# Performance work log

Hardware: AMD Instinct MI355X
Metric: run time of the kernel (lower is better)

Reference implementation:

```python
import jax, jax.numpy as jnp
import numpy as np

C = 256
HEADS = 4
HIDDEN = 4 * C  # LeFF default hidden_dim = dim*4
EPS = 1e-5


def conv2d(x, w, pad):
    # x: [B,C,H,W], w: [O,I,kh,kw]
    return jax.lax.conv_general_dilated(
        x, w, window_strides=(1, 1), padding=[(pad, pad), (pad, pad)],
        dimension_numbers=('NCHW', 'OIHW', 'NCHW'))


def dwconv2d(x, w, pad):
    # depthwise: w: [C,1,kh,kw], groups = C
    return jax.lax.conv_general_dilated(
        x, w, window_strides=(1, 1), padding=[(pad, pad), (pad, pad)],
        dimension_numbers=('NCHW', 'OIHW', 'NCHW'),
        feature_group_count=x.shape[1])


def conv1x1(x, w):
    # w: [O, I]; pointwise conv as einsum
    return jnp.einsum('oi,bihw->bohw', w, x)


def layernorm(x, weight, bias):
    # WithBias LayerNorm over channel dim of NCHW (matches to_3d -> LN over c)
    mu = jnp.mean(x, axis=1, keepdims=True)
    var = jnp.mean((x - mu) ** 2, axis=1, keepdims=True)
    xn = (x - mu) / jnp.sqrt(var + EPS)
    return xn * weight[None, :, None, None] + bias[None, :, None, None]


def mhsa(q, k, v, heads):
    # q,k,v: [B,C,H,W] -> global attention over N = H*W tokens
    b, c, h, w = q.shape
    d = c // heads
    scale = d ** -0.5
    def split(t):
        return t.reshape(b, heads, d, h * w)  # [B,H,d,N]
    qh, kh, vh = split(q), split(k), split(v)
    attn = jnp.einsum('bhdn,bhdm->bhnm', qh, kh) * scale  # [B,H,N,N]
    attn = jax.nn.softmax(attn, axis=-1)
    out = jnp.einsum('bhnm,bhdm->bhdn', attn, vh)
    return out.reshape(b, c, h, w)


def self_attn(x, w_qkv, w_proj, heads):
    qkv = conv1x1(x, w_qkv)  # [B,3C,H,W]
    q, k, v = jnp.split(qkv, 3, axis=1)
    return conv1x1(mhsa(q, k, v, heads), w_proj)


def cross_attn(qf, kvf, w_q, w_k, w_v, w_proj, heads):
    q = conv1x1(qf, w_q)
    k = conv1x1(kvf, w_k)
    v = conv1x1(kvf, w_v)
    return conv1x1(mhsa(q, k, v, heads), w_proj)


def leff(x, w_in, w_dw, w_out):
    h = conv1x1(x, w_in)
    h = dwconv2d(h, w_dw, pad=1)
    h = jax.nn.gelu(h, approximate=False)  # torch nn.GELU() = exact erf
    return conv1x1(h, w_out)


def setup_inputs() -> dict:
    key = jax.random.key(0)
    ks = jax.random.split(key, 32)
    s = 0.02
    inp = {
        'aop_feat': jax.random.normal(ks[0], (8, C, 32, 32), jnp.float32),
        'dop_feat': jax.random.normal(ks[1], (8, C, 32, 32), jnp.float32),
        'w_qconv': jax.random.normal(ks[2], (C, C, 3, 3), jnp.float32) * s,
        'w_kvconv': jax.random.normal(ks[3], (C, C, 5, 5), jnp.float32) * s,
        'lnq1_w': jnp.ones((C,), jnp.float32), 'lnq1_b': jnp.zeros((C,), jnp.float32),
        'lnkv1_w': jnp.ones((C,), jnp.float32), 'lnkv1_b': jnp.zeros((C,), jnp.float32),
        'lnq2_w': jnp.ones((C,), jnp.float32), 'lnq2_b': jnp.zeros((C,), jnp.float32),
        'lnkv2_w': jnp.ones((C,), jnp.float32), 'lnkv2_b': jnp.zeros((C,), jnp.float32),
        'lnffn_w': jnp.ones((C,), jnp.float32), 'lnffn_b': jnp.zeros((C,), jnp.float32),
        'saq_qkv': jax.random.normal(ks[4], (3 * C, C), jnp.float32) * s,
        'saq_proj': jax.random.normal(ks[5], (C, C), jnp.float32) * s,
        'sakv_qkv': jax.random.normal(ks[6], (3 * C, C), jnp.float32) * s,
        'sakv_proj': jax.random.normal(ks[7], (C, C), jnp.float32) * s,
        'ca_q': jax.random.normal(ks[8], (C, C), jnp.float32) * s,
        'ca_k': jax.random.normal(ks[9], (C, C), jnp.float32) * s,
        'ca_v': jax.random.normal(ks[10], (C, C), jnp.float32) * s,
        'ca_proj': jax.random.normal(ks[11], (C, C), jnp.float32) * s,
        'leff_in': jax.random.normal(ks[12], (HIDDEN, C), jnp.float32) * s,
        'leff_dw': jax.random.normal(ks[13], (HIDDEN, 1, 3, 3), jnp.float32) * s,
        'leff_out': jax.random.normal(ks[14], (C, HIDDEN), jnp.float32) * s,
    }
    return inp


def reference(aop_feat, dop_feat, w_qconv, w_kvconv,
              lnq1_w, lnq1_b, lnkv1_w, lnkv1_b, lnq2_w, lnq2_b,
              lnkv2_w, lnkv2_b, lnffn_w, lnffn_b,
              saq_qkv, saq_proj, sakv_qkv, sakv_proj,
              ca_q, ca_k, ca_v, ca_proj,
              leff_in, leff_dw, leff_out):
    # q branch
    q_branch = conv2d(aop_feat, w_qconv, pad=1)
    q_branch = q_branch + self_attn(layernorm(q_branch, lnq1_w, lnq1_b), saq_qkv, saq_proj, HEADS)
    q = layernorm(q_branch, lnq2_w, lnq2_b)
    # kv branch
    kv_branch = conv2d(dop_feat, w_kvconv, pad=2)
    kv_branch = kv_branch + self_attn(layernorm(kv_branch, lnkv1_w, lnkv1_b), sakv_qkv, sakv_proj, HEADS)
    kv = layernorm(kv_branch, lnkv2_w, lnkv2_b)
    # cross attention + FFN
    x = q_branch + cross_attn(q, kv, ca_q, ca_k, ca_v, ca_proj, HEADS)
    x = x + leff(layernorm(x, lnffn_w, lnffn_b), leff_in, leff_dw, leff_out)
    return x
```

## Files before the change

### kernel.cpp

```cpp
#include <hip/hip_runtime.h>
#include <hip/hip_bf16.h>


using bf16 = __hip_bfloat16;
typedef short v8s __attribute__((ext_vector_type(8)));
typedef float v4f  __attribute__((ext_vector_type(4)));

static __device__ __forceinline__ float bf2f(bf16 x) { return __bfloat162float(x); }
static __device__ __forceinline__ float us2f(unsigned short u)
{ union { unsigned int i; float f; } x; x.i = ((unsigned)u) << 16; return x.f; }
static __device__ __forceinline__ unsigned short f2us(float f)
{ bf16 h = __float2bfloat16(f); return *(unsigned short*)&h; }
static __device__ __forceinline__ float ldi(const void* p, size_t i, int isbf)
{ return isbf ? bf2f(((const bf16*)p)[i]) : ((const float*)p)[i]; }

__global__ void detect_kernel(const unsigned short* p, int* flag)
{
    if (threadIdx.x == 0 && blockIdx.x == 0)
        *flag = (p[0] == 0x3F80) ? 1 : 0;
}

struct CvtArgs { const void* src[20]; unsigned off[21]; };

__global__ __launch_bounds__(256) void pre_all(
    CvtArgs a,
    const void* __restrict__ s0, const void* __restrict__ s1,
    const void* __restrict__ W3, const void* __restrict__ W5,
    const void* __restrict__ Wdw, const int* __restrict__ flag,
    bf16* __restrict__ canon,
    bf16* __restrict__ d0, bf16* __restrict__ d1,
    bf16* __restrict__ R3, bf16* __restrict__ R5, bf16* __restrict__ Rdw)
{
    __shared__ float T[64][65];
    int bx = blockIdx.x, t = threadIdx.x;
    int isbf = *flag;
    if (bx < 5130) {
        unsigned e = bx * 256u + t;
        int s = 0;
        while (e >= a.off[s + 1]) ++s;
        canon[e] = __float2bfloat16(ldi(a.src[s], e - a.off[s], isbf));
    } else if (bx < 6154) {
        int i = bx - 5130;
        int x = i & 15, y = (i >> 4) & 3, z = i >> 6;
        const void* src = (z < 8) ? s0 : s1;
        bf16* dst       = (z < 8) ? d0 : d1;
        int hw0 = x * 64, c0 = y * 64, b = z & 7;
        int c = t >> 2, x16 = (t & 3) * 16;
        size_t sbase = ((size_t)b * 256 + c0 + c) * 1024 + hw0 + x16;
#pragma unroll
        for (int j = 0; j < 16; ++j) T[c][x16 + j] = ldi(src, sbase + j, isbf);
        __syncthreads();
        int hw = t >> 2, c16 = (t & 3) * 16;
        bf16* dp = dst + ((size_t)(b << 10) + hw0 + hw) * 256 + c0 + c16;
#pragma unroll
        for (int j = 0; j < 16; ++j) dp[j] = __float2bfloat16(T[c16 + j][hw]);
    } else {
        int idx = (bx - 6154) * 256 + t;
        if (idx < 589824) {
            int ci = idx & 255, o = (idx >> 8) & 255, khkw = idx >> 16;
            int kh = khkw / 3, kw = khkw % 3;
            R3[idx] = __float2bfloat16(
                ldi(W3, (((size_t)o * 256 + ci) * 3 + kh) * 3 + kw, isbf));
        } else if (idx < 2228224) {
            int j = idx - 589824;
            int ci = j & 255, o = (j >> 8) & 255, khkw = j >> 16;
            int kh = khkw / 5, kw = khkw % 5;
            R5[j] = __float2bfloat16(
                ldi(W5, (((size_t)o * 256 + ci) * 5 + kh) * 5 + kw, isbf));
        } else {
            int j = idx - 2228224;
            int c = j & 1023, tap = j >> 10;
            Rdw[j] = __float2bfloat16(ldi(Wdw, (size_t)c * 9 + tap, isbf));
        }
    }
}

static __device__ __forceinline__ void gemm_store(
    bf16* __restrict__ Yb, float* __restrict__ Yf, bf16* __restrict__ Y2,
    const bf16* __restrict__ R, int mode, int Ochan,
    int mm, int nn, float v)
{
    if (mode == 0) {
        size_t off = (size_t)mm * Ochan + nn;
        if (R) v += bf2f(R[off]);
        Yb[off] = __float2bfloat16(v);
    } else if (mode == 1) {
        Yb[((size_t)(nn >> 10) * Ochan + mm) * 1024 + (nn & 1023)] =
            __float2bfloat16(v);
    } else if (mode == 2) {
        Yf[((size_t)(nn >> 10) * Ochan + mm) * 1024 + (nn & 1023)] =
            v + bf2f(R[(size_t)nn * 256 + mm]);
    } else if (mode == 3) {
        if (mm < 512) Yb[(size_t)nn * 512 + mm] = __float2bfloat16(v);
        else Y2[((size_t)(nn >> 10) * 256 + (mm - 512)) * 1024 + (nn & 1023)] =
                 __float2bfloat16(v);
    } else {
        Yb[(size_t)nn * 512 + Ochan + mm] = __float2bfloat16(v);
    }
}

static __device__ __forceinline__ void mgemm_core(
    const short* __restrict__ MA, const short* __restrict__ MB,
    bf16* __restrict__ Yb, float* __restrict__ Yf, bf16* __restrict__ Y2,
    const bf16* __restrict__ R, int K, int mode, int Ochan,
    short As[64][72], short Bs[64][72])
{
    int m0 = blockIdx.x * 64, n0 = blockIdx.y * 64;
    int t = threadIdx.x, lane = t & 63, wv = t >> 6;
    int l15 = lane & 15, quad = lane >> 4;
    int srow = t >> 2, scol = (t & 3) * 16;

    const short* pa = &MA[(size_t)(m0 + srow) * K + scol];
    const short* pb = &MB[(size_t)(n0 + srow) * K + scol];

    v4f acc[4] = {};
    v8s ra0 = *(const v8s*)&pa[0], ra1 = *(const v8s*)&pa[8];
    v8s rb0 = *(const v8s*)&pb[0], rb1 = *(const v8s*)&pb[8];

    for (int k0 = 0; k0 < K; k0 += 64) {
        if (k0) __syncthreads();
        *(v8s*)&As[srow][scol]     = ra0;
        *(v8s*)&As[srow][scol + 8] = ra1;
        *(v8s*)&Bs[srow][scol]     = rb0;
        *(v8s*)&Bs[srow][scol + 8] = rb1;
        __syncthreads();
        if (k0 + 64 < K) {
            ra0 = *(const v8s*)&pa[k0 + 64];
            ra1 = *(const v8s*)&pa[k0 + 72];
            rb0 = *(const v8s*)&pb[k0 + 64];
            rb1 = *(const v8s*)&pb[k0 + 72];
        }
#pragma unroll
        for (int kk = 0; kk < 2; ++kk) {
            v8s a = *(const v8s*)&As[wv * 16 + l15][kk * 32 + quad * 8];
#pragma unroll
            for (int nt = 0; nt < 4; ++nt) {
                v8s b = *(const v8s*)&Bs[nt * 16 + l15][kk * 32 + quad * 8];
                acc[nt] = __builtin_amdgcn_mfma_f32_16x16x32_bf16(a, b, acc[nt], 0, 0, 0);
            }
        }
    }

#pragma unroll
    for (int nt = 0; nt < 4; ++nt)
#pragma unroll
        for (int r = 0; r < 4; ++r)
            gemm_store(Yb, Yf, Y2, R, mode, Ochan,
                       m0 + wv * 16 + quad * 4 + r,
                       n0 + nt * 16 + l15, acc[nt][r]);
}

__global__ __launch_bounds__(256) void mgemm(
    const short* __restrict__ MA, const short* __restrict__ MB,
    bf16* __restrict__ Yb, float* __restrict__ Yf, bf16* __restrict__ Y2,
    const bf16* __restrict__ R, int K, int mode, int Ochan)
{
    __shared__ short As[64][72], Bs[64][72];
    mgemm_core(MA, MB, Yb, Yf, Y2, R, K, mode, Ochan, As, Bs);
}

struct GA { const short* A; const short* B; bf16* Yb; float* Yf; bf16* Y2;
            const bf16* R; int K; int mode; int Oc; };
struct GA3 { GA g[3]; };

__global__ __launch_bounds__(256) void mgemm_z(GA3 P)
{
    __shared__ short As[64][72], Bs[64][72];
    const GA& a = P.g[blockIdx.z];
    mgemm_core(a.A, a.B, a.Yb, a.Yf, a.Y2, a.R, a.K, a.mode, a.Oc, As, Bs);
}

template <int KS, int PAD>
static __device__ __forceinline__ void mconv128_core(
    const short* __restrict__ Xn, const short* __restrict__ Wr,
    bf16* __restrict__ Y, float* __restrict__ Yf,
    short As[128][72], short Bs[128][72],
    int p0, int o0, int kbeg, int kend)
{
    int t = threadIdx.x, lane = t & 63, wv = t >> 6;
    int l15 = lane & 15, quad = lane >> 4;
    int wm = wv >> 1, wn = wv & 1;
    int srow = t >> 1, scol = (t & 1) * 32;

    int p  = p0 + srow;
    int hw = p & 1023, hh = hw >> 5, ww = hw & 31;
    size_t ib = ((size_t)(p >> 10)) << 10;

    v4f acc[4][4] = {};
    v8s ra[4], rb[4];

    auto ldk = [&](int k0) {
        int khkw = k0 >> 8;
        int kh = khkw / KS, kw = khkw % KS;
        int hi = hh + kh - PAD, wi = ww + kw - PAD;
        int aci = (k0 & 255) + scol;
        v8s z = {0, 0, 0, 0, 0, 0, 0, 0};
        ra[0] = z; ra[1] = z; ra[2] = z; ra[3] = z;
        if ((unsigned)hi < 32u && (unsigned)wi < 32u) {
            const short* sa = &Xn[(ib + (hi << 5) + wi) * 256 + aci];
            ra[0] = *(const v8s*)&sa[0];  ra[1] = *(const v8s*)&sa[8];
            ra[2] = *(const v8s*)&sa[16]; ra[3] = *(const v8s*)&sa[24];
        }
        const short* sb = &Wr[((size_t)khkw * 256 + o0 + srow) * 256 + (k0 & 255) + scol];
        rb[0] = *(const v8s*)&sb[0];  rb[1] = *(const v8s*)&sb[8];
        rb[2] = *(const v8s*)&sb[16]; rb[3] = *(const v8s*)&sb[24];
    };

    ldk(kbeg);

    for (int k0 = kbeg; k0 < kend; k0 += 64) {
        if (k0 != kbeg) __syncthreads();
        *(v8s*)&As[srow][scol]      = ra[0];
        *(v8s*)&As[srow][scol + 8]  = ra[1];
        *(v8s*)&As[srow][scol + 16] = ra[2];
        *(v8s*)&As[srow][scol + 24] = ra[3];
        *(v8s*)&Bs[srow][scol]      = rb[0];
        *(v8s*)&Bs[srow][scol + 8]  = rb[1];
        *(v8s*)&Bs[srow][scol + 16] = rb[2];
        *(v8s*)&Bs[srow][scol + 24] = rb[3];
        __syncthreads();
        if (k0 + 64 < kend) ldk(k0 + 64);
#pragma unroll
        for (int kk = 0; kk < 2; ++kk) {
            v8s af[4], bf[4];
#pragma unroll
            for (int i = 0; i < 4; ++i)
                af[i] = *(const v8s*)&As[wm * 64 + i * 16 + l15][kk * 32 + quad * 8];
#pragma unroll
            for (int i = 0; i < 4; ++i)
                bf[i] = *(const v8s*)&Bs[wn * 64 + i * 16 + l15][kk * 32 + quad * 8];
#pragma unroll
            for (int mt = 0; mt < 4; ++mt)
#pragma unroll
                for (int nt = 0; nt < 4; ++nt)
                    acc[mt][nt] = __builtin_amdgcn_mfma_f32_16x16x32_bf16(
                        af[mt], bf[nt], acc[mt][nt], 0, 0, 0);
        }
    }

#pragma unroll
    for (int mt = 0; mt < 4; ++mt)
#pragma unroll
        for (int nt = 0; nt < 4; ++nt)
#pragma unroll
            for (int r = 0; r < 4; ++r) {
                int pp = p0 + wm * 64 + mt * 16 + quad * 4 + r;
                int oo = o0 + wn * 64 + nt * 16 + l15;
                if (Yf) Yf[(size_t)pp * 256 + oo] = acc[mt][nt][r];
                else    Y[(size_t)pp * 256 + oo] = __float2bfloat16(acc[mt][nt][r]);
            }
}

__global__ __launch_bounds__(256) void mconv2(
    const short* __restrict__ Xa, const short* __restrict__ Wa, bf16* __restrict__ Ya,
    const short* __restrict__ Xb, const short* __restrict__ Wb,
    float* __restrict__ P0, float* __restrict__ P1, float* __restrict__ P2)
{
    __shared__ short As[128][72];
    __shared__ short Bs[128][72];
    int wg = blockIdx.x;
    if (wg < 128) {
        mconv128_core<3, 1>(Xa, Wa, Ya, nullptr, As, Bs,
                            (wg & 63) * 128, (wg >> 6) * 128, 0, 2304);
    } else {
        int j = wg - 128;
        int part = j >> 7, xy = j & 127;
        float* Pf = (part == 0) ? P0 : (part == 1) ? P1 : P2;
        int kbeg = part * 2112;
        int kend = (part < 2) ? kbeg + 2112 : 6400;
        mconv128_core<5, 2>(Xb, Wb, nullptr, Pf, As, Bs,
                            (xy & 63) * 128, (xy >> 6) * 128, kbeg, kend);
    }
}

__global__ __launch_bounds__(256) void addcvt3(
    const float* __restrict__ A, const float* __restrict__ B,
    const float* __restrict__ C, bf16* __restrict__ Y)
{
    int i = (blockIdx.x * 256 + threadIdx.x) * 4;
    float4 a = *(const float4*)&A[i];
    float4 b = *(const float4*)&B[i];
    float4 c = *(const float4*)&C[i];
    ushort4 o;
    o.x = f2us(a.x + b.x + c.x);
    o.y = f2us(a.y + b.y + c.y);
    o.z = f2us(a.z + b.z + c.z);
    o.w = f2us(a.w + b.w + c.w);
    *(ushort4*)((unsigned short*)Y + i) = o;
}

static __device__ __forceinline__ void attn_core(
    const bf16* __restrict__ QK, const bf16* __restrict__ V,
    bf16* __restrict__ Out, int b, int h, int n0,
    short Ks[64][72], short Vs[64][72])
{
    int t = threadIdx.x, lane = t & 63, wv = t >> 6;
    int l15 = lane & 15, quad = lane >> 4;
    int srow = t >> 2, scol = (t & 3) * 16;

    const short* qk = (const short*)QK;
    const short* vp = (const short*)V + ((size_t)b * 256 + h * 64) * 1024;

    size_t qrow = ((size_t)b * 1024 + n0 + wv * 16 + l15) * 512 + h * 64;
    v8s qf0 = *(const v8s*)&qk[qrow + quad * 8];
    v8s qf1 = *(const v8s*)&qk[qrow + 32 + quad * 8];

    v4f oacc[4] = {};
    float mi = -1e30f, li = 0.f, nmi = 0.f;
    const float SC = 0.18033688011112042f;

    int sig[4];
#pragma unroll
    for (int ct = 0; ct < 4; ++ct)
        sig[ct] = ((ct & 1) << 5) + ((l15 >> 2) << 3) + ((ct >> 1) << 2) + (l15 & 3);

    const short* kbase = &qk[((size_t)b * 1024 + srow) * 512 + 256 + h * 64 + scol];
    const short* vbase = vp + (size_t)srow * 1024 + scol;

    v8s rk0 = *(const v8s*)&kbase[0], rk1 = *(const v8s*)&kbase[8];
    v8s rv0 = *(const v8s*)&vbase[0], rv1 = *(const v8s*)&vbase[8];

    for (int m0 = 0; m0 < 1024; m0 += 64) {
        if (m0) __syncthreads();
        *(v8s*)&Ks[srow][scol]     = rk0;
        *(v8s*)&Ks[srow][scol + 8] = rk1;
        *(v8s*)&Vs[srow][scol]     = rv0;
        *(v8s*)&Vs[srow][scol + 8] = rv1;
        __syncthreads();
        if (m0 + 64 < 1024) {
            rk0 = *(const v8s*)&kbase[(size_t)(m0 + 64) * 512];
            rk1 = *(const v8s*)&kbase[(size_t)(m0 + 64) * 512 + 8];
            rv0 = *(const v8s*)&vbase[m0 + 64];
            rv1 = *(const v8s*)&vbase[m0 + 72];
        }

        v4f sacc[4];
        __builtin_amdgcn_s_setprio(1);
#pragma unroll
        for (int ct = 0; ct < 4; ++ct) {
            v8s kf0 = *(const v8s*)&Ks[sig[ct]][quad * 8];
            v8s kf1 = *(const v8s*)&Ks[sig[ct]][32 + quad * 8];
            v4f z = {0.f, 0.f, 0.f, 0.f};
            z = __builtin_amdgcn_mfma_f32_16x16x32_bf16(kf0, qf0, z, 0, 0, 0);
            z = __builtin_amdgcn_mfma_f32_16x16x32_bf16(kf1, qf1, z, 0, 0, 0);
            sacc[ct] = z;
        }
        __builtin_amdgcn_s_setprio(0);

        float pm = sacc[0][0];
#pragma unroll
        for (int ct = 0; ct < 4; ++ct)
#pragma unroll
            for (int r = 0; r < 4; ++r) pm = fmaxf(pm, sacc[ct][r]);
        if (__any(pm > mi)) {
            pm = fmaxf(pm, __shfl_xor(pm, 16));
            pm = fmaxf(pm, __shfl_xor(pm, 32));
            float mn = fmaxf(mi, pm);
            float al = exp2f((mi - mn) * SC);
            mi = mn;
            nmi = -mn * SC;
            li *= al;
#pragma unroll
            for (int dt = 0; dt < 4; ++dt)
#pragma unroll
                for (int r = 0; r < 4; ++r) oacc[dt][r] *= al;
        }

        short pv[4][4];
#pragma unroll
        for (int ct = 0; ct < 4; ++ct)
#pragma unroll
            for (int r = 0; r < 4; ++r) {
                float pvv = exp2f(fmaf(sacc[ct][r], SC, nmi));
                li += pvv;
                pv[ct][r] = (short)f2us(pvv);
            }

        v8s pf0 = {pv[0][0], pv[0][1], pv[0][2], pv[0][3],
                   pv[2][0], pv[2][1], pv[2][2], pv[2][3]};
        v8s pf1 = {pv[1][0], pv[1][1], pv[1][2], pv[1][3],
                   pv[3][0], pv[3][1], pv[3][2], pv[3][3]};

        __builtin_amdgcn_s_setprio(1);
#pragma unroll
        for (int dt = 0; dt < 4; ++dt) {
            v8s vf0 = *(const v8s*)&Vs[dt * 16 + l15][quad * 8];
            v8s vf1 = *(const v8s*)&Vs[dt * 16 + l15][32 + quad * 8];
            oacc[dt] = __builtin_amdgcn_mfma_f32_16x16x32_bf16(vf0, pf0, oacc[dt], 0, 0, 0);
            oacc[dt] = __builtin_amdgcn_mfma_f32_16x16x32_bf16(vf1, pf1, oacc[dt], 0, 0, 0);
        }
        __builtin_amdgcn_s_setprio(0);
    }

    li += __shfl_xor(li, 16);
    li += __shfl_xor(li, 32);
    float linv = 1.0f / li;

    size_t orow = ((size_t)b * 1024 + n0 + wv * 16 + l15) * 256 + h * 64;
#pragma unroll
    for (int dt = 0; dt < 4; ++dt) {
        ushort4 o;
        o.x = f2us(oacc[dt][0] * linv);
        o.y = f2us(oacc[dt][1] * linv);
        o.z = f2us(oacc[dt][2] * linv);
        o.w = f2us(oacc[dt][3] * linv);
        *(ushort4*)((unsigned short*)Out + orow + dt * 16 + quad * 4) = o;
    }
}

template <int NG>
__global__ __launch_bounds__(256) void attn_swz(
    const bf16* __restrict__ QK0, const bf16* __restrict__ V0, bf16* __restrict__ O0,
    const bf16* __restrict__ QK1, const bf16* __restrict__ V1, bf16* __restrict__ O1)
{
    __shared__ short Ks[64][72], Vs[64][72];
    int i = blockIdx.x;
    int xcd = i & 7, idx = i >> 3;
    int g = xcd * (NG / 8) + (idx >> 4);
    int n0 = (idx & 15) * 64;
    int h = g & 3, zz = g >> 2;
    int b = zz & 7;
    if (zz < 8) attn_core(QK0, V0, O0, b, h, n0, Ks, Vs);
    else        attn_core(QK1, V1, O1, b, h, n0, Ks, Vs);
}

static __device__ __forceinline__ void ln_row(
    const bf16* __restrict__ X, const bf16* __restrict__ g,
    const bf16* __restrict__ be, bf16* __restrict__ Y, size_t p)
{
    int lane = threadIdx.x & 63;
    const ushort4 u = *(const ushort4*)(X + p * 256 + lane * 4);
    float v0 = us2f(u.x), v1 = us2f(u.y), v2 = us2f(u.z), v3 = us2f(u.w);
    float s = v0 + v1 + v2 + v3;
    float ss = v0 * v0 + v1 * v1 + v2 * v2 + v3 * v3;
#pragma unroll
    for (int off = 32; off; off >>= 1) {
        s  += __shfl_xor(s, off);
        ss += __shfl_xor(ss, off);
    }
    float mu   = s * (1.0f / 256.0f);
    float var  = ss * (1.0f / 256.0f) - mu * mu;
    float rstd = rsqrtf(fmaxf(var, 0.0f) + 1e-5f);
    const ushort4 gu = *(const ushort4*)((const unsigned short*)g + lane * 4);
    const ushort4 bu = *(const ushort4*)((const unsigned short*)be + lane * 4);
    ushort4 o;
    o.x = f2us((v0 - mu) * rstd * us2f(gu.x) + us2f(bu.x));
    o.y = f2us((v1 - mu) * rstd * us2f(gu.y) + us2f(bu.y));
    o.z = f2us((v2 - mu) * rstd * us2f(gu.z) + us2f(bu.z));
    o.w = f2us((v3 - mu) * rstd * us2f(gu.w) + us2f(bu.w));
    *(ushort4*)(Y + p * 256 + lane * 4) = o;
}

__global__ __launch_bounds__(256) void ln_nhwc(
    const bf16* __restrict__ X, const bf16* __restrict__ g,
    const bf16* __restrict__ be, bf16* __restrict__ Y)
{
    int wv = threadIdx.x >> 6;
    ln_row(X, g, be, Y, (size_t)blockIdx.x * 4 + wv);
}

__global__ __launch_bounds__(256) void ln_nhwc2(
    const bf16* __restrict__ X0, const bf16* __restrict__ g0,
    const bf16* __restrict__ b0, bf16* __restrict__ Y0,
    const bf16* __restrict__ X1, const bf16* __restrict__ g1,
    const bf16* __restrict__ b1, bf16* __restrict__ Y1)
{
    int wv = threadIdx.x >> 6;
    int sel = blockIdx.x >> 11;
    size_t p = (size_t)(blockIdx.x & 2047) * 4 + wv;
    if (sel == 0) ln_row(X0, g0, b0, Y0, p);
    else          ln_row(X1, g1, b1, Y1, p);
}

__global__ __launch_bounds__(256) void dwgelu_nhwc(
    const bf16* __restrict__ H, const bf16* __restrict__ Wr,
    bf16* __restrict__ Y)
{
    int idx = blockIdx.x * 256 + threadIdx.x;
    int p = idx >> 7, c8 = (idx & 127) * 8;
    int hw = p & 1023, hh = hw >> 5, ww = hw & 31;
    size_t ib = ((size_t)(p >> 10)) << 10;
    float acc[8] = {};
#pragma unroll
    for (int kh = 0; kh < 3; ++kh)
#pragma unroll
        for (int kw = 0; kw < 3; ++kw) {
            int hi = hh + kh - 1, wi = ww + kw - 1;
            if ((unsigned)hi < 32u && (unsigned)wi < 32u) {
                v8s hv = *(const v8s*)((const short*)H + (ib + (hi << 5) + wi) * 1024 + c8);
                v8s wvv = *(const v8s*)((const short*)Wr + (kh * 3 + kw) * 1024 + c8);
#pragma unroll
                for (int j = 0; j < 8; ++j)
                    acc[j] = fmaf(us2f((unsigned short)wvv[j]),
                                  us2f((unsigned short)hv[j]), acc[j]);
            }
        }
    short ov[8];
#pragma unroll
    for (int j = 0; j < 8; ++j) {
        float x = acc[j];
        ov[j] = (short)f2us(0.5f * x * (1.0f + erff(x * 0.70710678118654752f)));
    }
    v8s o = {ov[0], ov[1], ov[2], ov[3], ov[4], ov[5], ov[6], ov[7]};
    *(v8s*)((short*)Y + (size_t)p * 1024 + c8) = o;
}

extern "C" void kernel_launch(void* const* d_in, const int* in_sizes, int n_in,
                              void* d_out, int out_size, void* d_ws, size_t ws_size,
                              hipStream_t stream)
{
    static const int  lidx[20] = {4,5,6,7,8,9,10,11,12,13,14,15,16,17,18,19,20,21,22,24};
    static const unsigned lsz[20] = {256,256,256,256,256,256,256,256,256,256,
                                     196608,65536,196608,65536,
                                     65536,65536,65536,65536,262144,262144};
    CvtArgs args;
    unsigned pre[21]; pre[0] = 0;
    for (int i = 0; i < 20; ++i) {
        args.src[i] = d_in[lidx[i]];
        pre[i + 1] = pre[i] + lsz[i];
    }
    for (int i = 0; i < 21; ++i) args.off[i] = pre[i];
    const unsigned ltot = pre[20];

    int*  flag  = (int*)d_ws;
    bf16* canon = (bf16*)d_ws + 128;
    bf16* cn[25];
    for (int i = 0; i < 20; ++i) cn[lidx[i]] = canon + pre[i];

    bf16* Wr3  = canon + ltot;
    bf16* Wr5  = Wr3 + 589824;
    bf16* Wdwr = Wr5 + 1638400;
    const size_t SZ = 2097152;
    bf16* slab = Wdwr + 9216;
    bf16* qb   = slab + 0 * SZ;
    bf16* kvb  = slab + 1 * SZ;
    bf16* t0   = slab + 2 * SZ;
    bf16* q    = slab + 3 * SZ;
    bf16* kv   = slab + 4 * SZ;
    bf16* QKb  = slab + 5 * SZ;
    bf16* Vb   = slab + 7 * SZ;
    bf16* t1   = slab + 8 * SZ;
    bf16* QK2  = slab + 9 * SZ;
    bf16* V2   = slab + 11 * SZ;
    bf16* aopT = slab + 9 * SZ;
    bf16* dopT = slab + 10 * SZ;
    bf16* hb   = slab + 3 * SZ;
    bf16* h2   = slab + 7 * SZ;
    float* P0f = (float*)(slab + 2 * SZ);
    float* P1f = (float*)(slab + 4 * SZ);
    float* P2f = (float*)(slab + 6 * SZ);
    float* out = (float*)d_out;

    dim3 blk(256);
    auto S = [](const bf16* p) { return (const short*)p; };

    detect_kernel<<<1, 64, 0, stream>>>((const unsigned short*)d_in[4], flag);
    pre_all<<<5130 + 1024 + 8740, blk, 0, stream>>>(
        args, d_in[0], d_in[1], d_in[2], d_in[3], d_in[23], flag,
        canon, aopT, dopT, Wr3, Wr5, Wdwr);

    mconv2<<<512, blk, 0, stream>>>(S(aopT), (const short*)Wr3, qb,
                                    S(dopT), (const short*)Wr5, P0f, P1f, P2f);
    addcvt3<<<2048, blk, 0, stream>>>(P0f, P1f, P2f, kvb);

    ln_nhwc2<<<4096, blk, 0, stream>>>(qb, cn[4], cn[5], t0,
                                       kvb, cn[6], cn[7], t1);
    GA3 P;
    P.g[0] = GA{S(cn[14]), S(t0), QKb, nullptr, Vb, nullptr, 256, 3, 0};
    P.g[1] = GA{S(cn[16]), S(t1), QK2, nullptr, V2, nullptr, 256, 3, 0};
    P.g[2] = P.g[1];
    mgemm_z<<<dim3(12, 128, 2), blk, 0, stream>>>(P);

    attn_swz<64><<<1024, blk, 0, stream>>>(QKb, Vb, t0, QK2, V2, t1);

    P.g[0] = GA{S(t0), S(cn[15]), qb, nullptr, nullptr, qb, 256, 0, 256};
    P.g[1] = GA{S(t1), S(cn[17]), kvb, nullptr, nullptr, kvb, 256, 0, 256};
    P.g[2] = P.g[1];
    mgemm_z<<<dim3(128, 4, 2), blk, 0, stream>>>(P);

    ln_nhwc2<<<4096, blk, 0, stream>>>(qb, cn[8], cn[9], q,
                                       kvb, cn[10], cn[11], kv);

    P.g[0] = GA{S(cn[18]), S(q),  QKb, nullptr, nullptr, nullptr, 256, 4, 0};
    P.g[1] = GA{S(cn[19]), S(kv), QKb, nullptr, nullptr, nullptr, 256, 4, 256};
    P.g[2] = GA{S(cn[20]), S(kv), Vb,  nullptr, nullptr, nullptr, 256, 1, 256};
    mgemm_z<<<dim3(4, 128, 3), blk, 0, stream>>>(P);

    attn_swz<32><<<512, blk, 0, stream>>>(QKb, Vb, t0, QKb, Vb, t0);
    mgemm<<<dim3(128, 4), blk, 0, stream>>>(S(t0), S(cn[21]), qb, nullptr, nullptr, qb, 256, 0, 256);

    ln_nhwc<<<2048, blk, 0, stream>>>(qb, cn[12], cn[13], t0);
    mgemm<<<dim3(128, 16), blk, 0, stream>>>(S(t0), S(cn[22]), hb, nullptr, nullptr, nullptr, 256, 0, 1024);
    dwgelu_nhwc<<<4096, blk, 0, stream>>>(hb, Wdwr, h2);
    mgemm<<<dim3(4, 128), blk, 0, stream>>>(S(cn[24]), S(h2), nullptr, out, nullptr, qb, 1024, 2, 256);
}
```

Measured before the change: 382.7 us.

## Split conv K-range evenly across more blocks and fuse partial sum into layernorm

The 3x3 conv now uses split-K over two halves and the 5x5 conv over four equal parts, giving 768 blocks instead of 512 for better load balance. Partials are written in bf16 instead of fp32, and the separate addcvt3 reduction kernel is removed. Partial summation now happens inside a new lnsum2 kernel that also writes the residual and applies layernorm, saving one launch and one pass over memory. Rounding partial sums to bf16 before adding them adds some numerical error.

Result: no change. 378.2 us, median of 2 (-1.2%).

```diff
diff --git a/kernel.cpp b/kernel.cpp
--- a/kernel.cpp
+++ b/kernel.cpp
@@ -252,41 +252,95 @@
 }
 
 __global__ __launch_bounds__(256) void mconv2(
-    const short* __restrict__ Xa, const short* __restrict__ Wa, bf16* __restrict__ Ya,
+    const short* __restrict__ Xa, const short* __restrict__ Wa,
+    bf16* __restrict__ Q0, bf16* __restrict__ Q1,
     const short* __restrict__ Xb, const short* __restrict__ Wb,
-    float* __restrict__ P0, float* __restrict__ P1, float* __restrict__ P2)
+    bf16* __restrict__ P0, bf16* __restrict__ P1,
+    bf16* __restrict__ P2, bf16* __restrict__ P3)
 {
     __shared__ short As[128][72];
     __shared__ short Bs[128][72];
     int wg = blockIdx.x;
-    if (wg < 128) {
-        mconv128_core<3, 1>(Xa, Wa, Ya, nullptr, As, Bs,
-                            (wg & 63) * 128, (wg >> 6) * 128, 0, 2304);
+    if (wg < 256) {
+        int half = wg >> 7, xy = wg & 127;
+        bf16* Y = half ? Q1 : Q0;
+        mconv128_core<3, 1>(Xa, Wa, Y, nullptr, As, Bs,
+                            (xy & 63) * 128, (xy >> 6) * 128,
+                            half * 1152, half * 1152 + 1152);
     } else {
-        int j = wg - 128;
+        int j = wg - 256;
         int part = j >> 7, xy = j & 127;
-        float* Pf = (part == 0) ? P0 : (part == 1) ? P1 : P2;
-        int kbeg = part * 2112;
-        int kend = (part < 2) ? kbeg + 2112 : 6400;
-        mconv128_core<5, 2>(Xb, Wb, nullptr, Pf, As, Bs,
-                            (xy & 63) * 128, (xy >> 6) * 128, kbeg, kend);
-    }
-}
-
-__global__ __launch_bounds__(256) void addcvt3(
-    const float* __restrict__ A, const float* __restrict__ B,
-    const float* __restrict__ C, bf16* __restrict__ Y)
-{
-    int i = (blockIdx.x * 256 + threadIdx.x) * 4;
-    float4 a = *(const float4*)&A[i];
-    float4 b = *(const float4*)&B[i];
-    float4 c = *(const float4*)&C[i];
-    ushort4 o;
-    o.x = f2us(a.x + b.x + c.x);
-    o.y = f2us(a.y + b.y + c.y);
-    o.z = f2us(a.z + b.z + c.z);
-    o.w = f2us(a.w + b.w + c.w);
-    *(ushort4*)((unsigned short*)Y + i) = o;
+        bf16* Y = (part == 0) ? P0 : (part == 1) ? P1 : (part == 2) ? P2 : P3;
+        mconv128_core<5, 2>(Xb, Wb, Y, nullptr, As, Bs,
+                            (xy & 63) * 128, (xy >> 6) * 128,
+                            part * 1600, part * 1600 + 1600);
+    }
+}
+
+static __device__ __forceinline__ void ln_vals(
+    float v0, float v1, float v2, float v3,
+    const bf16* __restrict__ g, const bf16* __restrict__ be,
+    bf16* __restrict__ Y, size_t off, int lane)
+{
+    float s = v0 + v1 + v2 + v3;
+    float ss = v0 * v0 + v1 * v1 + v2 * v2 + v3 * v3;
+#pragma unroll
+    for (int o = 32; o; o >>= 1) {
+        s  += __shfl_xor(s, o);
+        ss += __shfl_xor(ss, o);
+    }
+    float mu   = s * (1.0f / 256.0f);
+    float var  = ss * (1.0f / 256.0f) - mu * mu;
+    float rstd = rsqrtf(fmaxf(var, 0.0f) + 1e-5f);
+    const ushort4 gu = *(const ushort4*)((const unsigned short*)g + lane * 4);
+    const ushort4 bu = *(const ushort4*)((const unsigned short*)be + lane * 4);
+    ushort4 o4;
+    o4.x = f2us((v0 - mu) * rstd * us2f(gu.x) + us2f(bu.x));
+    o4.y = f2us((v1 - mu) * rstd * us2f(gu.y) + us2f(bu.y));
+    o4.z = f2us((v2 - mu) * rstd * us2f(gu.z) + us2f(bu.z));
+    o4.w = f2us((v3 - mu) * rstd * us2f(gu.w) + us2f(bu.w));
+    *(ushort4*)((unsigned short*)Y + off) = o4;
+}
+
+__global__ __launch_bounds__(256) void lnsum2(
+    const bf16* __restrict__ Q0, const bf16* __restrict__ Q1,
+    const bf16* __restrict__ g0, const bf16* __restrict__ b0,
+    bf16* __restrict__ qb, bf16* __restrict__ Y0,
+    const bf16* __restrict__ P0, const bf16* __restrict__ P1,
+    const bf16* __restrict__ P2, const bf16* __restrict__ P3,
+    const bf16* __restrict__ g1, const bf16* __restrict__ b1,
+    bf16* __restrict__ kvb, bf16* __restrict__ Y1)
+{
+    int wv = threadIdx.x >> 6, lane = threadIdx.x & 63;
+    int sel = blockIdx.x >> 11;
+    size_t p = (size_t)(blockIdx.x & 2047) * 4 + wv;
+    size_t off = p * 256 + lane * 4;
+    float v0, v1, v2, v3;
+    if (sel == 0) {
+        ushort4 a = *(const ushort4*)((const unsigned short*)Q0 + off);
+        ushort4 b = *(const ushort4*)((const unsigned short*)Q1 + off);
+        v0 = us2f(a.x) + us2f(b.x);
+        v1 = us2f(a.y) + us2f(b.y);
+        v2 = us2f(a.z) + us2f(b.z);
+        v3 = us2f(a.w) + us2f(b.w);
+        ushort4 s;
+        s.x = f2us(v0); s.y = f2us(v1); s.z = f2us(v2); s.w = f2us(v3);
+        *(ushort4*)((unsigned short*)qb + off) = s;
+        ln_vals(v0, v1, v2, v3, g0, b0, Y0, off, lane);
+    } else {
+        ushort4 a = *(const ushort4*)((const unsigned short*)P0 + off);
+        ushort4 b = *(const ushort4*)((const unsigned short*)P1 + off);
+        ushort4 c = *(const ushort4*)((const unsigned short*)P2 + off);
+        ushort4 d = *(const ushort4*)((const unsigned short*)P3 + off);
+        v0 = us2f(a.x) + us2f(b.x) + us2f(c.x) + us2f(d.x);
+        v1 = us2f(a.y) + us2f(b.y) + us2f(c.y) + us2f(d.y);
+        v2 = us2f(a.z) + us2f(b.z) + us2f(c.z) + us2f(d.z);
+        v3 = us2f(a.w) + us2f(b.w) + us2f(c.w) + us2f(d.w);
+        ushort4 s;
+        s.x = f2us(v0); s.y = f2us(v1); s.z = f2us(v2); s.w = f2us(v3);
+        *(ushort4*)((unsigned short*)kvb + off) = s;
+        ln_vals(v0, v1, v2, v3, g1, b1, Y1, off, lane);
+    }
 }
 
 static __device__ __forceinline__ void attn_core(
@@ -431,24 +485,7 @@
     int lane = threadIdx.x & 63;
     const ushort4 u = *(const ushort4*)(X + p * 256 + lane * 4);
     float v0 = us2f(u.x), v1 = us2f(u.y), v2 = us2f(u.z), v3 = us2f(u.w);
-    float s = v0 + v1 + v2 + v3;
-    float ss = v0 * v0 + v1 * v1 + v2 * v2 + v3 * v3;
-#pragma unroll
-    for (int off = 32; off; off >>= 1) {
-        s  += __shfl_xor(s, off);
-        ss += __shfl_xor(ss, off);
-    }
-    float mu   = s * (1.0f / 256.0f);
-    float var  = ss * (1.0f / 256.0f) - mu * mu;
-    float rstd = rsqrtf(fmaxf(var, 0.0f) + 1e-5f);
-    const ushort4 gu = *(const ushort4*)((const unsigned short*)g + lane * 4);
-    const ushort4 bu = *(const ushort4*)((const unsigned short*)be + lane * 4);
-    ushort4 o;
-    o.x = f2us((v0 - mu) * rstd * us2f(gu.x) + us2f(bu.x));
-    o.y = f2us((v1 - mu) * rstd * us2f(gu.y) + us2f(bu.y));
-    o.z = f2us((v2 - mu) * rstd * us2f(gu.z) + us2f(bu.z));
-    o.w = f2us((v3 - mu) * rstd * us2f(gu.w) + us2f(bu.w));
-    *(ushort4*)(Y + p * 256 + lane * 4) = o;
+    ln_vals(v0, v1, v2, v3, g, be, Y, p * 256 + lane * 4, lane);
 }
 
 __global__ __launch_bounds__(256) void ln_nhwc(
@@ -546,9 +583,12 @@
     bf16* dopT = slab + 10 * SZ;
     bf16* hb   = slab + 3 * SZ;
     bf16* h2   = slab + 7 * SZ;
-    float* P0f = (float*)(slab + 2 * SZ);
-    float* P1f = (float*)(slab + 4 * SZ);
-    float* P2f = (float*)(slab + 6 * SZ);
+    bf16* Q0p  = slab + 2 * SZ;
+    bf16* Q1p  = slab + 3 * SZ;
+    bf16* Pp0  = slab + 4 * SZ;
+    bf16* Pp1  = slab + 5 * SZ;
+    bf16* Pp2  = slab + 6 * SZ;
+    bf16* Pp3  = slab + 7 * SZ;
     float* out = (float*)d_out;
 
     dim3 blk(256);
@@ -559,12 +599,13 @@
         args, d_in[0], d_in[1], d_in[2], d_in[3], d_in[23], flag,
         canon, aopT, dopT, Wr3, Wr5, Wdwr);
 
-    mconv2<<<512, blk, 0, stream>>>(S(aopT), (const short*)Wr3, qb,
-                                    S(dopT), (const short*)Wr5, P0f, P1f, P2f);
-    addcvt3<<<2048, blk, 0, stream>>>(P0f, P1f, P2f, kvb);
-
-    ln_nhwc2<<<4096, blk, 0, stream>>>(qb, cn[4], cn[5], t0,
-                                       kvb, cn[6], cn[7], t1);
+    mconv2<<<768, blk, 0, stream>>>(S(aopT), (const short*)Wr3, Q0p, Q1p,
+                                    S(dopT), (const short*)Wr5,
+                                    Pp0, Pp1, Pp2, Pp3);
+
+    lnsum2<<<4096, blk, 0, stream>>>(Q0p, Q1p, cn[4], cn[5], qb, t0,
+                                     Pp0, Pp1, Pp2, Pp3, cn[6], cn[7], kvb, t1);
+
     GA3 P;
     P.g[0] = GA{S(cn[14]), S(t0), QKb, nullptr, Vb, nullptr, 256, 3, 0};
     P.g[1] = GA{S(cn[16]), S(t1), QK2, nullptr, V2, nullptr, 256, 3, 0};
```
